# Optimization experiments

Hardware: AMD Instinct MI355X
Metric: run time of the kernel (lower is better)

The kernel has to match this reference:

```python
import jax, jax.numpy as jnp
import numpy as np
from jax import lax

FEAT_STRIDE = 16
PRE_NMS_TOPN = 2000
POST_NMS_TOPN = 300
NMS_THRESH = 0.7
MIN_SIZE = 16.0
IMG_H, IMG_W = 1600.0, 2400.0


def _generate_anchors(base_size=16, ratios=(0.5, 1.0, 2.0), scales=(8, 16, 32)):
    w = h = float(base_size)
    xc = yc = 0.5 * (base_size - 1)
    size = w * h
    out = []
    for r in ratios:
        ws = np.round(np.sqrt(size / r))
        hs = np.round(ws * r)
        for s in scales:
            W, H = ws * s, hs * s
            out.append([xc - 0.5 * (W - 1), yc - 0.5 * (H - 1),
                        xc + 0.5 * (W - 1), yc + 0.5 * (H - 1)])
    return np.array(out, dtype=np.float32)  # [9,4]

ANCHORS = jnp.asarray(_generate_anchors())


def _conv(x, w, b, padding):
    y = lax.conv_general_dilated(x, w, (1, 1), padding,
                                 dimension_numbers=('NCHW', 'OIHW', 'NCHW'))
    return y + b[None, :, None, None]


def _nms_mask(boxes, thresh):
    # greedy NMS over score-sorted boxes; returns keep mask
    N = boxes.shape[0]
    x1, y1, x2, y2 = boxes[:, 0], boxes[:, 1], boxes[:, 2], boxes[:, 3]
    areas = (x2 - x1 + 1.0) * (y2 - y1 + 1.0)
    idx = jnp.arange(N)

    def body(i, supp):
        xx1 = jnp.maximum(x1[i], x1)
        yy1 = jnp.maximum(y1[i], y1)
        xx2 = jnp.minimum(x2[i], x2)
        yy2 = jnp.minimum(y2[i], y2)
        w = jnp.maximum(xx2 - xx1 + 1.0, 0.0)
        h = jnp.maximum(yy2 - yy1 + 1.0, 0.0)
        inter = w * h
        iou = inter / (areas[i] + areas - inter)
        cond = (iou > thresh) & (idx > i) & jnp.logical_not(supp[i])
        return supp | cond

    supp = lax.fori_loop(0, N, body, jnp.zeros((N,), dtype=bool))
    return jnp.logical_not(supp)


def reference(features, conv1_w, conv1_b, score_w, score_b, bbox_w, bbox_b, img_info):
    # RPN head
    x = jax.nn.relu(_conv(features, conv1_w, conv1_b, 'SAME'))
    cls = _conv(x, score_w, score_b, 'VALID')    # [1, 2A, H, W]
    deltas = _conv(x, bbox_w, bbox_b, 'VALID')   # [1, 4A, H, W]
    N, C, H, W = cls.shape
    A = C // 2
    # reshape_layer to [N,2,A*H,W], softmax over dim 1, reshape back
    prob = jax.nn.softmax(cls.reshape(N, 2, A * H, W), axis=1).reshape(N, C, H, W)
    fg = prob[:, A:, :, :]                                  # foreground probs
    scores = fg.transpose(0, 2, 3, 1).reshape(-1)           # (H*W*A,)
    d = deltas.transpose(0, 2, 3, 1).reshape(-1, 4)         # (H*W*A, 4)

    # anchor grid (h-major, w-minor, anchor-minor) matching the transpose order
    shift_x = jnp.arange(W, dtype=jnp.float32) * FEAT_STRIDE
    shift_y = jnp.arange(H, dtype=jnp.float32) * FEAT_STRIDE
    sx, sy = jnp.meshgrid(shift_x, shift_y)                 # [H,W]
    shifts = jnp.stack([sx.ravel(), sy.ravel(), sx.ravel(), sy.ravel()], axis=1)
    anchors = (ANCHORS[None, :, :] + shifts[:, None, :]).reshape(-1, 4)

    # bbox_transform_inv decode
    ws = anchors[:, 2] - anchors[:, 0] + 1.0
    hs = anchors[:, 3] - anchors[:, 1] + 1.0
    cx = anchors[:, 0] + 0.5 * ws
    cy = anchors[:, 1] + 0.5 * hs
    pcx = d[:, 0] * ws + cx
    pcy = d[:, 1] * hs + cy
    pw = jnp.exp(d[:, 2]) * ws
    ph = jnp.exp(d[:, 3]) * hs
    props = jnp.stack([pcx - 0.5 * pw, pcy - 0.5 * ph,
                       pcx + 0.5 * pw, pcy + 0.5 * ph], axis=1)
    # clip to image
    props = jnp.stack([jnp.clip(props[:, 0], 0.0, img_info[1] - 1.0),
                       jnp.clip(props[:, 1], 0.0, img_info[0] - 1.0),
                       jnp.clip(props[:, 2], 0.0, img_info[1] - 1.0),
                       jnp.clip(props[:, 3], 0.0, img_info[0] - 1.0)], axis=1)

    # min-size filter (masked, jit-friendly)
    bw = props[:, 2] - props[:, 0] + 1.0
    bh = props[:, 3] - props[:, 1] + 1.0
    min_sz = MIN_SIZE * img_info[2]
    valid = (bw >= min_sz) & (bh >= min_sz)
    scores = jnp.where(valid, scores, -jnp.inf)

    # pre-NMS top-k (sorted desc)
    top_scores, order = lax.top_k(scores, PRE_NMS_TOPN)
    boxes = props[order]
    keep = _nms_mask(boxes, NMS_THRESH)
    kept_scores = jnp.where(keep, top_scores, -jnp.inf)
    post_scores, kidx = lax.top_k(kept_scores, POST_NMS_TOPN)
    final = boxes[kidx]
    rois = jnp.concatenate([jnp.zeros((POST_NMS_TOPN, 1), final.dtype), final], axis=1)
    return rois, post_scores


def setup_inputs() -> dict:
    key = jax.random.key(0)
    ks = jax.random.split(key, 4)
    H, W = 100, 150  # 1600x2400 image at stride 16
    features = jax.random.normal(ks[0], (1, 512, H, W), dtype=jnp.float32)
    conv1_w = jax.random.normal(ks[1], (512, 512, 3, 3), dtype=jnp.float32) * 0.01
    conv1_b = jnp.zeros((512,), dtype=jnp.float32)
    score_w = jax.random.normal(ks[2], (18, 512, 1, 1), dtype=jnp.float32) * 0.01
    score_b = jnp.zeros((18,), dtype=jnp.float32)
    bbox_w = jax.random.normal(ks[3], (36, 512, 1, 1), dtype=jnp.float32) * 0.001
    bbox_b = jnp.zeros((36,), dtype=jnp.float32)
    img_info = jnp.array([IMG_H, IMG_W, 1.0], dtype=jnp.float32)
    return {"features": features, "conv1_w": conv1_w, "conv1_b": conv1_b,
            "score_w": score_w, "score_b": score_b,
            "bbox_w": bbox_w, "bbox_b": bbox_b, "img_info": img_info}
```

## Files before the change

kernel.cpp:

```cpp
#include <hip/hip_runtime.h>
#include <math.h>

#define Hh 100
#define Ww 150
#define Mm 15000
#define NP 135000

typedef double f64x4 __attribute__((ext_vector_type(4)));

#if defined(__HIP_DEVICE_COMPILE__)
#if __has_builtin(__builtin_amdgcn_mfma_f64_16x16x4f64)
#define MFMA64(a,b,c) __builtin_amdgcn_mfma_f64_16x16x4f64((a),(b),(c),0,0,0)
#elif __has_builtin(__builtin_amdgcn_mfma_f64_16x16x4_f64)
#define MFMA64(a,b,c) __builtin_amdgcn_mfma_f64_16x16x4_f64((a),(b),(c),0,0,0)
#else
#error "no f64 mfma builtin on device"
#endif
#define GLOAD4(g,l) __builtin_amdgcn_global_load_lds( \
    (const __attribute__((address_space(1))) unsigned*)(g), \
    (__attribute__((address_space(3))) unsigned*)(l), 4, 0, 0)
#else
#define MFMA64(a,b,c) (c)
#define GLOAD4(g,l) ((void)(g),(void)(l))
#endif

__constant__ double ANCH[9][4] = {
  {-84.0,-40.0,99.0,55.0},{-176.0,-88.0,191.0,103.0},{-360.0,-184.0,375.0,191.0},
  {-56.0,-56.0,71.0,71.0},{-120.0,-120.0,135.0,135.0},{-248.0,-248.0,263.0,263.0},
  {-36.0,-80.0,51.0,95.0},{-80.0,-168.0,95.0,183.0},{-168.0,-344.0,183.0,359.0}};

__global__ __launch_bounds__(256) void prep_wT(const float* __restrict__ w,
                                               float* __restrict__ wT) {
  __shared__ float t[32][32][10];
  const int co0 = blockIdx.x * 32, ci0 = blockIdx.y * 32;
  for (int e = threadIdx.x; e < 9216; e += 256) {
    int cr = e / 288;
    int rem = e - cr * 288;
    int cir = rem / 9, tap = rem - cir * 9;
    t[cir][cr][tap] = w[(size_t)(co0 + cr) * 4608 + (ci0 + cir) * 9 + tap];
  }
  __syncthreads();
  for (int e = threadIdx.x; e < 9216; e += 256) {
    int tap = e / 1024;
    int rem = e - tap * 1024;
    int cir = rem >> 5, cr = rem & 31;
    wT[(size_t)tap * 262144 + (size_t)(ci0 + cir) * 512 + (co0 + cr)] = t[cir][cr][tap];
  }
}

__global__ void prep_w54(const float* __restrict__ sw, const float* __restrict__ bw,
                         double* __restrict__ w54) {
  int idx = blockIdx.x * 256 + threadIdx.x;
  if (idx < 54 * 512) {
    int o = idx >> 9, c = idx & 511;
    w54[idx] = (double)((o < 18) ? sw[o * 512 + c] : bw[(o - 18) * 512 + c]);
  }
}

__global__ __launch_bounds__(256, 4) void conv3x3(const float* __restrict__ feat,
                                                  const float* __restrict__ wT,
                                                  const float* __restrict__ bias,
                                                  float* __restrict__ x) {
  __shared__ union {
    struct { float A[2][32][72]; float B[2][32][136]; } s;
    float Lx[128][65];
  } sm;
  const int tid = threadIdx.x;
  const int lane = tid & 63;
  const int wv = tid >> 6;
  const int pxw = wv * 16;
  const int m0 = blockIdx.x * 64;
  const int n0 = blockIdx.y * 128;
  const int l15 = lane & 15, l4 = lane >> 4;

  f64x4 zero; zero[0] = 0.0; zero[1] = 0.0; zero[2] = 0.0; zero[3] = 0.0;
  f64x4 acc[8];
#pragma unroll
  for (int q = 0; q < 8; ++q) acc[q] = zero;

  const int ka = wv * 8;
  const int ma = m0 + lane;
  const int ha = ma / 150, wa = ma - ha * 150;

  auto stage = [&](int cn, int buf) {
    const int tap = cn >> 4;
    const int cb = (cn & 15) << 5;
    const int t3 = tap / 3;
    const int dy = t3 - 1, dx = tap - t3 * 3 - 1;
    const int hh = ha + dy, wwp = wa + dx;
    const bool ok = (ma < Mm) && (hh >= 0) && (hh < Hh) && (wwp >= 0) && (wwp < Ww);
    if (!ok) {
#pragma unroll
      for (int kk = 0; kk < 8; ++kk) sm.s.A[buf][ka + kk][lane] = 0.0f;
    } else {
      const float* ab = feat + (size_t)(cb + ka) * Mm + (hh * Ww + wwp);
#pragma unroll
      for (int kk = 0; kk < 8; ++kk)
        GLOAD4(ab + (size_t)kk * Mm, &sm.s.A[buf][ka + kk][0]);
    }
    const float* wbase = wT + (size_t)tap * 262144 + (size_t)(cb + ka) * 512 + n0 + lane;
#pragma unroll
    for (int kk = 0; kk < 8; ++kk) {
      GLOAD4(wbase + (size_t)kk * 512,      &sm.s.B[buf][ka + kk][0]);
      GLOAD4(wbase + (size_t)kk * 512 + 64, &sm.s.B[buf][ka + kk][64]);
    }
  };

  stage(0, 0);
  __syncthreads();

  for (int c = 0; c < 144; ++c) {
    const int b = c & 1;
    if (c + 1 < 144) stage(c + 1, b ^ 1);
#pragma unroll
    for (int t = 0; t < 8; ++t) {
      const int kt = t * 4 + l4;
      const double a = (double)sm.s.A[b][kt][pxw + l15];
#pragma unroll
      for (int q = 0; q < 8; ++q) {
        const double bq = (double)sm.s.B[b][kt][q * 16 + l15];
        acc[q] = MFMA64(a, bq, acc[q]);
      }
    }
    __syncthreads();
  }

  const double ap1 = (l4 == 0) ? (double)l15 : 0.0;
  const double bp1 = (l4 == 0) ? 1.0 : 0.0;
  const f64x4 rowp = MFMA64(ap1, bp1, zero);
  const double ap2 = (l4 == 0) ? 1.0 : 0.0;
  const double bp2 = (l4 == 0) ? (double)l15 : 0.0;
  const f64x4 colp = MFMA64(ap2, bp2, zero);

#pragma unroll
  for (int q = 0; q < 8; ++q)
#pragma unroll
    for (int r = 0; r < 4; ++r) {
      const int row = pxw + (int)rowp[r];
      const int col = q * 16 + (int)colp[r];
      const double v = acc[q][r] + (double)bias[n0 + col];
      sm.Lx[col][row] = (float)(v > 0.0 ? v : 0.0);
    }
  __syncthreads();
  for (int e = tid; e < 64 * 128; e += 256) {
    const int co = e >> 6, p = e & 63;
    const int m = m0 + p;
    if (m < Mm) x[(size_t)(n0 + co) * Mm + m] = sm.Lx[co][p];
  }
}

__global__ __launch_bounds__(256) void conv1x1(const float* __restrict__ x,
                                               const double* __restrict__ w54,
                                               const float* __restrict__ sb,
                                               const float* __restrict__ bb,
                                               float* __restrict__ cls,
                                               float* __restrict__ dl) {
  int m = blockIdx.x * 256 + threadIdx.x;
  int g = blockIdx.y;
  double acc[9];
#pragma unroll
  for (int o = 0; o < 9; ++o) acc[o] = 0.0;
  if (m < Mm) {
    const double* wg = w54 + (size_t)g * 9 * 512;
    for (int c = 0; c < 512; ++c) {
      double v = (double)x[(size_t)c * Mm + m];
#pragma unroll
      for (int o = 0; o < 9; ++o) acc[o] += v * wg[o * 512 + c];
    }
#pragma unroll
    for (int o = 0; o < 9; ++o) {
      int oo = g * 9 + o;
      if (oo < 18) cls[oo * Mm + m] = (float)(acc[o] + (double)sb[oo]);
      else dl[(oo - 18) * Mm + m] = (float)(acc[o] + (double)bb[oo - 18]);
    }
  }
}

__global__ void decode(const float* __restrict__ cls, const float* __restrict__ dl,
                       const float* __restrict__ info, double4* __restrict__ props,
                       float* __restrict__ scoresF, unsigned long long* __restrict__ keys64,
                       unsigned* __restrict__ keys32, unsigned* __restrict__ hist) {
  int i = blockIdx.x * 256 + threadIdx.x;
  if (i >= NP) return;
  int m = i / 9, a = i - m * 9;
  int h = m / 150, w = m - h * 150;
  double c0 = (double)cls[a * Mm + m], c1 = (double)cls[(9 + a) * Mm + m];
  double mx = fmax(c0, c1);
  double e0 = exp(c0 - mx), e1 = exp(c1 - mx);
  double p = e1 / (e0 + e1);
  double d0 = (double)dl[(a * 4 + 0) * Mm + m], d1 = (double)dl[(a * 4 + 1) * Mm + m];
  double d2 = (double)dl[(a * 4 + 2) * Mm + m], d3 = (double)dl[(a * 4 + 3) * Mm + m];
  double sx = (double)w * 16.0, sy = (double)h * 16.0;
  double ax1 = ANCH[a][0] + sx, ay1 = ANCH[a][1] + sy;
  double ax2 = ANCH[a][2] + sx, ay2 = ANCH[a][3] + sy;
  double aw = ax2 - ax1 + 1.0, ah = ay2 - ay1 + 1.0;
  double cx = ax1 + 0.5 * aw, cy = ay1 + 0.5 * ah;
  double pcx = d0 * aw + cx, pcy = d1 * ah + cy;
  double pw = exp(d2) * aw, ph = exp(d3) * ah;
  double x1 = pcx - 0.5 * pw, y1 = pcy - 0.5 * ph;
  double x2 = pcx + 0.5 * pw, y2 = pcy + 0.5 * ph;
  double IH = (double)info[0], IW = (double)info[1], sc = (double)info[2];
  x1 = fmin(fmax(x1, 0.0), IW - 1.0); y1 = fmin(fmax(y1, 0.0), IH - 1.0);
  x2 = fmin(fmax(x2, 0.0), IW - 1.0); y2 = fmin(fmax(y2, 0.0), IH - 1.0);
  double bwd = x2 - x1 + 1.0, bhd = y2 - y1 + 1.0;
  bool valid = (bwd >= 16.0 * sc) && (bhd >= 16.0 * sc);
  double score = valid ? p : -__builtin_inf();
  double4 pr; pr.x = x1; pr.y = y1; pr.z = x2; pr.w = y2;
  props[i] = pr;
  float pf = (float)score;
  scoresF[i] = pf;
  unsigned long long b = (unsigned long long)__double_as_longlong(score);
  unsigned long long s = (b >> 63) ? ~b : (b | 0x8000000000000000ull);
  unsigned long long k = ~s;
  keys64[i] = (k & ~0x3FFFFull) | (unsigned long long)i;
  unsigned ub = __float_as_uint(pf);
  unsigned us = (ub >> 31) ? ~ub : (ub | 0x80000000u);
  unsigned k32 = ~us;
  keys32[i] = k32;
  atomicAdd(&hist[k32 >> 16], 1u);
}

__global__ __launch_bounds__(1024) void cutoff_k(const unsigned* __restrict__ hist,
                                                 int* __restrict__ Bout) {
  __shared__ unsigned ps[1024];
  int t = threadIdx.x;
  unsigned s = 0;
  for (int b = t * 64; b < t * 64 + 64; ++b) s += hist[b];
  ps[t] = s; __syncthreads();
  for (int off = 1; off < 1024; off <<= 1) {
    unsigned a = ps[t];
    unsigned bb2 = (t >= off) ? ps[t - off] : 0u;
    __syncthreads();
    ps[t] = a + bb2;
    __syncthreads();
  }
  unsigned excl = ps[t] - s;
  if (excl < 2000u) {
    unsigned run = excl;
    for (int b = t * 64; b < t * 64 + 64; ++b) {
      unsigned nb = run + hist[b];
      if (run < 2000u && nb >= 2000u) *Bout = b;
      run = nb;
    }
  }
}

__global__ void compact_k(const unsigned* __restrict__ keys32,
                          const unsigned long long* __restrict__ keys64,
                          const int* __restrict__ Bptr,
                          unsigned long long* __restrict__ cand, int* __restrict__ cnt) {
  int i = blockIdx.x * 256 + threadIdx.x;
  if (i >= NP) return;
  int B = *Bptr;
  if ((int)(keys32[i] >> 16) <= B) {
    int pos = atomicAdd(cnt, 1);
    if (pos < 8192) cand[pos] = keys64[i];
  }
}

__global__ __launch_bounds__(1024) void sort_top(const unsigned long long* __restrict__ cand,
                                                 const int* __restrict__ pcnt,
                                                 const double4* __restrict__ props,
                                                 const float* __restrict__ scoresF,
                                                 double4* __restrict__ boxes2000,
                                                 float* __restrict__ score2000) {
  __shared__ unsigned long long sh[8192];
  int t = threadIdx.x;
  int cnt = *pcnt; if (cnt > 8192) cnt = 8192;
  for (int i = t; i < 8192; i += 1024) sh[i] = (i < cnt) ? cand[i] : ~0ull;
  __syncthreads();
  for (int kb = 1; kb <= 13; ++kb) {
    int k = 1 << kb;
    for (int jb = kb - 1; jb >= 0; --jb) {
      int j = 1 << jb;
      for (int s = t; s < 4096; s += 1024) {
        int i = ((s >> jb) << (jb + 1)) | (s & (j - 1));
        int l = i + j;
        bool up = ((i & k) == 0);
        unsigned long long a = sh[i], b = sh[l];
        if (up ? (a > b) : (a < b)) { sh[i] = b; sh[l] = a; }
      }
      __syncthreads();
    }
  }
  for (int r = t; r < 2000; r += 1024) {
    unsigned long long key = sh[r];
    int idx = (int)(key & 0x3FFFFull);
    boxes2000[r] = props[idx];
    score2000[r] = scoresF[idx];
  }
}

__global__ __launch_bounds__(256) void nms_mask(const double4* __restrict__ boxes,
                                                unsigned long long* __restrict__ mask) {
  int tid = threadIdx.x;
  int r = blockIdx.x * 8 + (tid >> 5);
  int wd = tid & 31;
  double4 bi = boxes[r];
  double ai = (bi.z - bi.x + 1.0) * (bi.w - bi.y + 1.0);
  unsigned long long bits = 0;
  int j0 = wd * 64;
  int jmax = 2000 - j0; if (jmax > 64) jmax = 64;
  for (int jj = 0; jj < jmax; ++jj) {
    int j = j0 + jj;
    if (j > r) {
      double4 bj = boxes[j];
      double xx1 = fmax(bi.x, bj.x), yy1 = fmax(bi.y, bj.y);
      double xx2 = fmin(bi.z, bj.z), yy2 = fmin(bi.w, bj.w);
      double w_ = fmax(xx2 - xx1 + 1.0, 0.0), h_ = fmax(yy2 - yy1 + 1.0, 0.0);
      double inter = w_ * h_;
      double aj = (bj.z - bj.x + 1.0) * (bj.w - bj.y + 1.0);
      double iou = inter / (ai + aj - inter);
      if (iou > 0.7) bits |= 1ull << jj;
    }
  }
  mask[r * 32 + wd] = bits;
}

__global__ __launch_bounds__(256) void suppress(const unsigned long long* __restrict__ mask,
                                                unsigned long long* __restrict__ aliveOut) {
  __shared__ unsigned long long rows[64][32];
  int tid = threadIdx.x;
  int lane = tid & 63;
  unsigned long long myword = 0;
  if (tid < 64) {
    if (lane < 31) myword = ~0ull;
    else if (lane == 31) myword = 0xFFFFull;
  }
  for (int c = 0; c < 32; ++c) {
    __syncthreads();
    for (int idx = tid; idx < 2048; idx += 256) {
      int g = c * 2048 + idx;
      ((unsigned long long*)rows)[idx] = (g < 64000) ? mask[g] : 0ull;
    }
    __syncthreads();
    if (tid < 64) {
      for (int r = 0; r < 64; ++r) {
        int i = c * 64 + r;
        unsigned long long rw = rows[r][lane & 31];
        unsigned long long aw = __shfl(myword, i >> 6);
        if ((aw >> (i & 63)) & 1ull) {
          if (lane < 32) myword &= ~rw;
        }
      }
    }
  }
  __syncthreads();
  if (tid < 32) aliveOut[tid] = myword;
}

__global__ __launch_bounds__(1024) void finalize(const unsigned long long* __restrict__ alive,
                                                 const double4* __restrict__ boxes,
                                                 const float* __restrict__ scores,
                                                 float* __restrict__ out) {
  __shared__ int ps[1024];
  int t = threadIdx.x;
  int e0 = 2 * t, e1 = 2 * t + 1;
  int f0 = (e0 < 2000) ? (int)((alive[e0 >> 6] >> (e0 & 63)) & 1ull) : 0;
  int f1 = (e1 < 2000) ? (int)((alive[e1 >> 6] >> (e1 & 63)) & 1ull) : 0;
  int v = f0 + f1;
  ps[t] = v; __syncthreads();
  for (int off = 1; off < 1024; off <<= 1) {
    int a = ps[t];
    int b = (t >= off) ? ps[t - off] : 0;
    __syncthreads();
    ps[t] = a + b;
    __syncthreads();
  }
  int incl = ps[t];
  int excl = incl - v;
  int Na = ps[1023];
  if (f0 && excl < 300) {
    double4 bx = boxes[e0];
    out[excl * 5 + 0] = 0.f; out[excl * 5 + 1] = (float)bx.x; out[excl * 5 + 2] = (float)bx.y;
    out[excl * 5 + 3] = (float)bx.z; out[excl * 5 + 4] = (float)bx.w;
    out[1500 + excl] = scores[e0];
  }
  int p1 = excl + f0;
  if (f1 && p1 < 300) {
    double4 bx = boxes[e1];
    out[p1 * 5 + 0] = 0.f; out[p1 * 5 + 1] = (float)bx.x; out[p1 * 5 + 2] = (float)bx.y;
    out[p1 * 5 + 3] = (float)bx.z; out[p1 * 5 + 4] = (float)bx.w;
    out[1500 + p1] = scores[e1];
  }
  if (Na < 300) {
    if (e0 < 2000 && !f0) {
      int q = Na + (e0 - excl);
      if (q < 300) {
        double4 bx = boxes[e0];
        out[q * 5 + 0] = 0.f; out[q * 5 + 1] = (float)bx.x; out[q * 5 + 2] = (float)bx.y;
        out[q * 5 + 3] = (float)bx.z; out[q * 5 + 4] = (float)bx.w;
        out[1500 + q] = -__builtin_inff();
      }
    }
    if (e1 < 2000 && !f1) {
      int q = Na + (e1 - (excl + f0));
      if (q < 300) {
        double4 bx = boxes[e1];
        out[q * 5 + 0] = 0.f; out[q * 5 + 1] = (float)bx.x; out[q * 5 + 2] = (float)bx.y;
        out[q * 5 + 3] = (float)bx.z; out[q * 5 + 4] = (float)bx.w;
        out[1500 + q] = -__builtin_inff();
      }
    }
  }
}

extern "C" void kernel_launch(void* const* d_in, const int* in_sizes, int n_in,
                              void* d_out, int out_size, void* d_ws, size_t ws_size,
                              hipStream_t stream) {
  (void)in_sizes; (void)n_in; (void)out_size; (void)ws_size;
  const float* feat = (const float*)d_in[0];
  const float* w1   = (const float*)d_in[1];
  const float* b1   = (const float*)d_in[2];
  const float* sw   = (const float*)d_in[3];
  const float* sb   = (const float*)d_in[4];
  const float* bw   = (const float*)d_in[5];
  const float* bb   = (const float*)d_in[6];
  const float* info = (const float*)d_in[7];
  float* out = (float*)d_out;

  char* ws = (char*)d_ws;
  size_t off = 0;
  auto alloc = [&](size_t bytes) -> void* {
    void* p = ws + off;
    off += (bytes + 255) & ~(size_t)255;
    return p;
  };
  float* x        = (float*)alloc((size_t)512 * Mm * 4);
  float* wT       = (float*)alloc((size_t)9 * 512 * 512 * 4);
  double* w54     = (double*)alloc((size_t)54 * 512 * 8);
  float* cls      = (float*)alloc((size_t)18 * Mm * 4);
  float* dl       = (float*)alloc((size_t)36 * Mm * 4);
  double4* props  = (double4*)alloc((size_t)NP * 32);
  float* scoresF  = (float*)alloc((size_t)NP * 4);
  unsigned long long* keys64 = (unsigned long long*)alloc((size_t)NP * 8);
  unsigned* keys32 = (unsigned*)alloc((size_t)NP * 4);
  unsigned* hist   = (unsigned*)alloc((size_t)65536 * 4);
  int* Bptr        = (int*)alloc(256);
  int* cnt         = (int*)alloc(256);
  unsigned long long* cand = (unsigned long long*)alloc((size_t)8192 * 8);
  double4* boxes2000 = (double4*)alloc((size_t)2000 * 32);
  float* score2000   = (float*)alloc((size_t)2000 * 4);
  unsigned long long* mask  = (unsigned long long*)alloc((size_t)2000 * 32 * 8);
  unsigned long long* alive = (unsigned long long*)alloc((size_t)32 * 8);

  hipMemsetAsync(hist, 0, 65536 * 4, stream);
  hipMemsetAsync(cnt, 0, 4, stream);

  prep_wT<<<dim3(16, 16), 256, 0, stream>>>(w1, wT);
  prep_w54<<<108, 256, 0, stream>>>(sw, bw, w54);
  conv3x3<<<dim3(235, 4), 256, 0, stream>>>(feat, wT, b1, x);
  conv1x1<<<dim3(59, 6), 256, 0, stream>>>(x, w54, sb, bb, cls, dl);
  decode<<<528, 256, 0, stream>>>(cls, dl, info, props, scoresF, keys64, keys32, hist);
  cutoff_k<<<1, 1024, 0, stream>>>(hist, Bptr);
  compact_k<<<528, 256, 0, stream>>>(keys32, keys64, Bptr, cand, cnt);
  sort_top<<<1, 1024, 0, stream>>>(cand, cnt, props, scoresF, boxes2000, score2000);
  nms_mask<<<250, 256, 0, stream>>>(boxes2000, mask);
  suppress<<<1, 256, 0, stream>>>(mask, alive);
  finalize<<<1, 1024, 0, stream>>>(alive, boxes2000, score2000, out);
}
```

Before: 2.001 ms.

## Tile conv3x3 spatially with halo so one input load serves all nine taps

The 3x3 conv now gives each block a 2x32 pixel tile with a 4x34 halo. It stages each 32-channel slab of input once into shared memory and reuses it across all nine taps, instead of reloading a shifted input tile for every tap. Weights are loaded with plain float4 loads in place of the async global_load_lds path, and the two-buffer pipelining is removed, so loads no longer overlap with MFMA work. It also adds more barriers per tap and wastes work on padded columns (160 computed vs 150 real).

```diff
diff --git a/kernel.cpp b/kernel.cpp
--- a/kernel.cpp
+++ b/kernel.cpp
@@ -16,12 +16,8 @@
 #else
 #error "no f64 mfma builtin on device"
 #endif
-#define GLOAD4(g,l) __builtin_amdgcn_global_load_lds( \
-    (const __attribute__((address_space(1))) unsigned*)(g), \
-    (__attribute__((address_space(3))) unsigned*)(l), 4, 0, 0)
 #else
 #define MFMA64(a,b,c) (c)
-#define GLOAD4(g,l) ((void)(g),(void)(l))
 #endif
 
 __constant__ double ANCH[9][4] = {
@@ -62,15 +58,17 @@
                                                   const float* __restrict__ bias,
                                                   float* __restrict__ x) {
   __shared__ union {
-    struct { float A[2][32][72]; float B[2][32][136]; } s;
+    struct { float A[32][136]; float B[32][136]; } s;
     float Lx[128][65];
   } sm;
   const int tid = threadIdx.x;
   const int lane = tid & 63;
   const int wv = tid >> 6;
-  const int pxw = wv * 16;
-  const int m0 = blockIdx.x * 64;
-  const int n0 = blockIdx.y * 128;
+  const int rp = wv >> 1;
+  const int cpb = (wv & 1) * 16;
+  const int r0 = blockIdx.x;
+  const int c0 = blockIdx.y;
+  const int n0 = blockIdx.z * 128;
   const int l15 = lane & 15, l4 = lane >> 4;
 
   f64x4 zero; zero[0] = 0.0; zero[1] = 0.0; zero[2] = 0.0; zero[3] = 0.0;
@@ -78,51 +76,39 @@
 #pragma unroll
   for (int q = 0; q < 8; ++q) acc[q] = zero;
 
-  const int ka = wv * 8;
-  const int ma = m0 + lane;
-  const int ha = ma / 150, wa = ma - ha * 150;
-
-  auto stage = [&](int cn, int buf) {
-    const int tap = cn >> 4;
-    const int cb = (cn & 15) << 5;
-    const int t3 = tap / 3;
-    const int dy = t3 - 1, dx = tap - t3 * 3 - 1;
-    const int hh = ha + dy, wwp = wa + dx;
-    const bool ok = (ma < Mm) && (hh >= 0) && (hh < Hh) && (wwp >= 0) && (wwp < Ww);
-    if (!ok) {
-#pragma unroll
-      for (int kk = 0; kk < 8; ++kk) sm.s.A[buf][ka + kk][lane] = 0.0f;
-    } else {
-      const float* ab = feat + (size_t)(cb + ka) * Mm + (hh * Ww + wwp);
-#pragma unroll
-      for (int kk = 0; kk < 8; ++kk)
-        GLOAD4(ab + (size_t)kk * Mm, &sm.s.A[buf][ka + kk][0]);
-    }
-    const float* wbase = wT + (size_t)tap * 262144 + (size_t)(cb + ka) * 512 + n0 + lane;
-#pragma unroll
-    for (int kk = 0; kk < 8; ++kk) {
-      GLOAD4(wbase + (size_t)kk * 512,      &sm.s.B[buf][ka + kk][0]);
-      GLOAD4(wbase + (size_t)kk * 512 + 64, &sm.s.B[buf][ka + kk][64]);
-    }
-  };
-
-  stage(0, 0);
-  __syncthreads();
-
-  for (int c = 0; c < 144; ++c) {
-    const int b = c & 1;
-    if (c + 1 < 144) stage(c + 1, b ^ 1);
-#pragma unroll
-    for (int t = 0; t < 8; ++t) {
-      const int kt = t * 4 + l4;
-      const double a = (double)sm.s.A[b][kt][pxw + l15];
-#pragma unroll
-      for (int q = 0; q < 8; ++q) {
-        const double bq = (double)sm.s.B[b][kt][q * 16 + l15];
-        acc[q] = MFMA64(a, bq, acc[q]);
+  const int cq = tid & 31, kb = (tid >> 5) * 4;
+  const int hb = 2 * r0 - 1, wb = 32 * c0 - 1;
+
+  for (int cb = 0; cb < 512; cb += 32) {
+    for (int e = tid; e < 4352; e += 256) {
+      int k = e / 136, rc = e - k * 136;
+      int r = rc / 34, cc = rc - r * 34;
+      int hg = hb + r, wg = wb + cc;
+      bool ok = (hg >= 0) && (hg < Hh) && (wg >= 0) && (wg < Ww);
+      sm.s.A[k][rc] = ok ? feat[(size_t)(cb + k) * Mm + hg * Ww + wg] : 0.0f;
+    }
+    for (int tap = 0; tap < 9; ++tap) {
+      const int t3 = tap / 3;
+      const int dy = t3 - 1, dx = tap - t3 * 3 - 1;
+      const float* wbp = wT + (size_t)tap * 262144 + n0;
+#pragma unroll
+      for (int kk = 0; kk < 4; ++kk)
+        *(float4*)&sm.s.B[kb + kk][cq * 4] =
+            *(const float4*)&wbp[(size_t)(cb + kb + kk) * 512 + cq * 4];
+      __syncthreads();
+      const int aoff = (rp + 1 + dy) * 34 + (cpb + 1 + dx);
+#pragma unroll
+      for (int t = 0; t < 8; ++t) {
+        const int kt = t * 4 + l4;
+        const double a = (double)sm.s.A[kt][aoff + l15];
+#pragma unroll
+        for (int q = 0; q < 8; ++q) {
+          const double bq = (double)sm.s.B[kt][q * 16 + l15];
+          acc[q] = MFMA64(a, bq, acc[q]);
+        }
       }
-    }
-    __syncthreads();
+      __syncthreads();
+    }
   }
 
   const double ap1 = (l4 == 0) ? (double)l15 : 0.0;
@@ -136,16 +122,16 @@
   for (int q = 0; q < 8; ++q)
 #pragma unroll
     for (int r = 0; r < 4; ++r) {
-      const int row = pxw + (int)rowp[r];
+      const int p = rp * 32 + cpb + (int)rowp[r];
       const int col = q * 16 + (int)colp[r];
       const double v = acc[q][r] + (double)bias[n0 + col];
-      sm.Lx[col][row] = (float)(v > 0.0 ? v : 0.0);
+      sm.Lx[col][p] = (float)(v > 0.0 ? v : 0.0);
     }
   __syncthreads();
   for (int e = tid; e < 64 * 128; e += 256) {
     const int co = e >> 6, p = e & 63;
-    const int m = m0 + p;
-    if (m < Mm) x[(size_t)(n0 + co) * Mm + m] = sm.Lx[co][p];
+    const int h = 2 * r0 + (p >> 5), w = 32 * c0 + (p & 31);
+    if (w < Ww) x[(size_t)(n0 + co) * Mm + h * Ww + w] = sm.Lx[co][p];
   }
 }
 
@@ -449,7 +435,7 @@
 
   prep_wT<<<dim3(16, 16), 256, 0, stream>>>(w1, wT);
   prep_w54<<<108, 256, 0, stream>>>(sw, bw, w54);
-  conv3x3<<<dim3(235, 4), 256, 0, stream>>>(feat, wT, b1, x);
+  conv3x3<<<dim3(50, 5, 4), 256, 0, stream>>>(feat, wT, b1, x);
   conv1x1<<<dim3(59, 6), 256, 0, stream>>>(x, w54, sb, bb, cls, dl);
   decode<<<528, 256, 0, stream>>>(cls, dl, info, props, scoresF, keys64, keys32, hist);
   cutoff_k<<<1, 1024, 0, stream>>>(hist, Bptr);
```

New measurement: 1.967 ms. Within noise of the previous version (-1.7%).
